# Kernel optimization log

Measured on AMD Instinct MI355X. Metric: run time of the kernel, lower is better.

The kernel has to match this reference:

```python
import jax, jax.numpy as jnp
import numpy as np

B, N, K, C = 4, 4096, 32, 192  # batch, npoint, nsample, channels (C % 6 == 0)
EPS = 1e-5


def setup_inputs() -> dict:
    key = jax.random.key(0)
    ks = jax.random.split(key, 8)
    p = jax.random.normal(ks[0], (B, N, 3), jnp.float32)
    x = jax.random.normal(ks[1], (B, C, N), jnp.float32)
    idx = jax.random.randint(ks[2], (B, N, K), 0, N)  # ball-query neighbor ids
    W = jax.random.normal(ks[3], (C, C + 3), jnp.float32) * 0.05  # 1x1 conv weight
    gamma = 1.0 + 0.1 * jax.random.normal(ks[4], (C,), jnp.float32)
    beta = 0.1 * jax.random.normal(ks[5], (C,), jnp.float32)
    rmean = 0.1 * jax.random.normal(ks[6], (C,), jnp.float32)
    rvar = jax.random.uniform(ks[7], (C,), jnp.float32) + 0.5  # positive running var
    return dict(p=p, x=x, idx=idx, W=W, gamma=gamma, beta=beta, rmean=rmean, rvar=rvar)


def reference(p, x, idx, W, gamma, beta, rmean, rvar):
    # --- grouper: gather neighbors, relative coords ---
    pn = jax.vmap(lambda pp, ii: pp[ii])(p, idx)            # [B,N,K,3]
    dp = jnp.transpose(pn - p[:, :, None, :], (0, 3, 1, 2))  # [B,3,N,K]
    xj = jax.vmap(lambda xx, ii: xx[:, ii])(x, idx)          # [B,C,N,K]
    # --- PosPool sin/cos positional embedding fused with features ---
    feat_dim = C // 6
    dim_mat = jnp.power(500.0, jnp.arange(feat_dim, dtype=jnp.float32) / feat_dim)
    div = (50.0 * dp)[..., None] / dim_mat                   # [B,3,N,K,fd]
    pe = jnp.concatenate([jnp.sin(div), jnp.cos(div)], axis=-1)  # [B,3,N,K,2fd]
    pe = jnp.transpose(pe, (0, 1, 4, 2, 3)).reshape(B, C, N, K)  # [B,C,N,K]
    agg = xj * pe + pe
    # --- dp_fj concat -> 1x1 conv -> BN(eval) -> ReLU ---
    h = jnp.concatenate([dp, agg], axis=1)                   # [B,C+3,N,K]
    y = jnp.einsum('oc,bcnk->bonk', W, h)                    # [B,C,N,K]
    inv = gamma / jnp.sqrt(rvar + EPS)
    y = y * inv[:, None, None] + (beta - rmean * inv)[:, None, None]
    y = jax.nn.relu(y)
    # --- max reduction over neighbors ---
    return jnp.max(y, axis=-1)                               # [B,C,N]
```

## Files before the change

kernel.cpp:

```cpp
#include <hip/hip_runtime.h>
#include <math.h>

#define B_   4
#define N_   4096
#define K_   32
#define C_   192
#define CH_  195
#define KPAD 224
#define PTS  2
#define NKT  7
#define NNT  4
#define GRID ((B_ * N_) / PTS)

using half8  = __attribute__((ext_vector_type(8))) _Float16;
using half2v = __attribute__((ext_vector_type(2))) _Float16;
using f32x4  = __attribute__((ext_vector_type(4))) float;

__device__ _Float16 g_Wp[C_ * KPAD];
__device__ _Float16 g_xT[(size_t)B_ * N_ * C_];

__device__ __forceinline__ float dpp_max16(float v) {
    int s;
    s = __builtin_amdgcn_update_dpp(0, __float_as_int(v), 0xB1,  0xF, 0xF, true);
    v = fmaxf(v, __int_as_float(s));
    s = __builtin_amdgcn_update_dpp(0, __float_as_int(v), 0x4E,  0xF, 0xF, true);
    v = fmaxf(v, __int_as_float(s));
    s = __builtin_amdgcn_update_dpp(0, __float_as_int(v), 0x141, 0xF, 0xF, true);
    v = fmaxf(v, __int_as_float(s));
    s = __builtin_amdgcn_update_dpp(0, __float_as_int(v), 0x140, 0xF, 0xF, true);
    v = fmaxf(v, __int_as_float(s));
    return v;
}

__global__ __launch_bounds__(256) void prep(const float* __restrict__ x,
                                            const float* __restrict__ W,
                                            const float* __restrict__ gamma_,
                                            const float* __restrict__ rvar) {
    const int tid = threadIdx.x;
    if (blockIdx.x < 512) {
        __shared__ float s[32][201];
        const int b  = blockIdx.x >> 7;
        const int n0 = (blockIdx.x & 127) * 32;
        const int cl = tid >> 3;
        const int n4 = (tid & 7) * 4;
#pragma unroll
        for (int it = 0; it < 6; ++it) {
            const int c = it * 32 + cl;
            const float4 v = *(const float4*)(x + ((size_t)b * C_ + c) * N_ + n0 + n4);
            s[n4 + 0][c] = v.x; s[n4 + 1][c] = v.y; s[n4 + 2][c] = v.z; s[n4 + 3][c] = v.w;
        }
        __syncthreads();
        const int n  = tid >> 3;
        const int og = tid & 7;
#pragma unroll
        for (int it = 0; it < 3; ++it) {
            const int oc = it * 8 + og;
            half8 v;
#pragma unroll
            for (int jj = 0; jj < 8; ++jj) v[jj] = (_Float16)s[n][oc * 8 + jj];
            *(half8*)(g_xT + ((size_t)b * N_ + n0 + n) * C_ + oc * 8) = v;
        }
    } else {
        const int i = (blockIdx.x - 512) * 256 + tid;
        if (i < C_ * KPAD) {
            const int o = i / KPAD, r = i - o * KPAD;
            const float inv = gamma_[o] * rsqrtf(rvar[o] + 1e-5f);
            float v = 0.0f;
            if (r < 3)                  v = W[o * CH_ + r];
            else if (r >= 8 && r < 200) v = W[o * CH_ + 3 + (r - 8)];
            g_Wp[i] = (_Float16)(v * inv);
        }
    }
}

__global__ __launch_bounds__(256, 5) void la_mfma(
    const float* __restrict__ p,
    const int*   __restrict__ idx,
    const float* __restrict__ gamma_,
    const float* __restrict__ beta_,
    const float* __restrict__ rmean,
    const float* __restrict__ rvar,
    float* __restrict__ out)
{
    __shared__ _Float16 hb[NKT * NNT * 64 * 8];
    __shared__ float s_bias[C_], s_fr[32];

    const int tid  = threadIdx.x;
    const int lane = tid & 63;
    const int w    = tid >> 6;
    const int l15  = lane & 15;
    const int quad = lane >> 4;

    const int q  = blockIdx.x & 7;
    const int sI = blockIdx.x >> 3;
    const int L  = q * (GRID / 8) + sI;
    const int bn0 = L * PTS;
    const int b   = bn0 >> 12;
    const int n0  = bn0 & (N_ - 1);

    if (tid < C_) {
        const float inv = gamma_[tid] * rsqrtf(rvar[tid] + 1e-5f);
        s_bias[tid] = beta_[tid] - rmean[tid] * inv;
    }
    if (tid < 32) s_fr[tid] = 7.9577471546f * exp2f(-(float)tid * 0.2801808715263400f);
    __syncthreads();

    {
        const int col = w * 16 + l15;
        const int pt  = col >> 5;
        const int k   = col & 31;
        const int gp  = bn0 + pt;
        const int j   = idx[(size_t)gp * K_ + k];
        const float d0 = p[(size_t)(b * N_ + j) * 3 + 0] - p[(size_t)gp * 3 + 0];
        const float d1 = p[(size_t)(b * N_ + j) * 3 + 1] - p[(size_t)gp * 3 + 1];
        const float d2 = p[(size_t)(b * N_ + j) * 3 + 2] - p[(size_t)gp * 3 + 2];
        const _Float16* xh = g_xT + ((size_t)b * N_ + j) * C_;

        float sfr[8];
#pragma unroll
        for (int jj = 0; jj < 8; ++jj) sfr[jj] = s_fr[quad * 8 + jj];

#pragma unroll
        for (int i6 = 0; i6 < 6; ++i6) {
            const int chunk = quad + 4 * i6;
            const half8 v = *(const half8*)(xh + chunk * 8);
            const float dd  = (chunk < 8) ? d0 : ((chunk < 16) ? d1 : d2);
            const float off = (chunk & 4) ? 0.25f : 0.0f;
            half8 hv;
#pragma unroll
            for (int jj = 0; jj < 8; jj += 2) {
                const float pe0 = __builtin_amdgcn_sinf(fmaf(dd, sfr[jj],     off));
                const float pe1 = __builtin_amdgcn_sinf(fmaf(dd, sfr[jj + 1], off));
                const half2v pe2 = __builtin_bit_cast(half2v, __builtin_amdgcn_cvt_pkrtz(pe0, pe1));
                half2v v2; v2[0] = v[jj]; v2[1] = v[jj + 1];
                const half2v r2 = pe2 * v2 + pe2;
                hv[jj] = r2[0]; hv[jj + 1] = r2[1];
            }
            const int ro = chunk + 1;
            const int kt = ro >> 2, kq = ro & 3;
            *(half8*)(&hb[(size_t)((kt * NNT + w) * 64 + kq * 16 + l15) * 8]) = hv;
        }
        if (quad == 0) {
            half8 hv0 = (half8)(_Float16)0.0f;
            hv0[0] = (_Float16)d0; hv0[1] = (_Float16)d1; hv0[2] = (_Float16)d2;
            *(half8*)(&hb[(size_t)((0 * NNT + w) * 64 + 0 * 16 + l15) * 8]) = hv0;
        } else {
            const int ro = 24 + quad;
            const int kt = ro >> 2, kq = ro & 3;
            *(half8*)(&hb[(size_t)((kt * NNT + w) * 64 + kq * 16 + l15) * 8]) = (half8)(_Float16)0.0f;
        }
    }
    __syncthreads();

    f32x4 acc[3][4];
#pragma unroll
    for (int i = 0; i < 3; ++i)
#pragma unroll
        for (int t = 0; t < 4; ++t) acc[i][t] = (f32x4)0.0f;

#pragma unroll
    for (int kt = 0; kt < NKT; ++kt) {
        const int k0 = kt * 32 + quad * 8;
        half8 a[3], bf[4];
#pragma unroll
        for (int i = 0; i < 3; ++i) {
            const int m = (w * 3 + i) * 16 + l15;
            a[i] = *(const half8*)(g_Wp + (size_t)m * KPAD + k0);
        }
#pragma unroll
        for (int t = 0; t < 4; ++t)
            bf[t] = *(const half8*)(&hb[(size_t)((kt * NNT + t) * 64 + lane) * 8]);
#pragma unroll
        for (int i = 0; i < 3; ++i)
#pragma unroll
            for (int t = 0; t < 4; ++t)
                acc[i][t] = __builtin_amdgcn_mfma_f32_16x16x32_f16(a[i], bf[t], acc[i][t], 0, 0, 0);
    }

#pragma unroll
    for (int i = 0; i < 3; ++i) {
        const int mbase = (w * 3 + i) * 16 + quad * 4;
#pragma unroll
        for (int r = 0; r < 4; ++r) {
            float v0 = fmaxf(acc[i][0][r], acc[i][1][r]);
            float v1 = fmaxf(acc[i][2][r], acc[i][3][r]);
            v0 = dpp_max16(v0);
            v1 = dpp_max16(v1);
            if (l15 == 0) {
                const int m = mbase + r;
                const float bias = s_bias[m];
                float2 o2;
                o2.x = fmaxf(v0 + bias, 0.0f);
                o2.y = fmaxf(v1 + bias, 0.0f);
                *(float2*)(&out[((size_t)b * C_ + m) * N_ + n0]) = o2;
            }
        }
    }
}

extern "C" void kernel_launch(void* const* d_in, const int* in_sizes, int n_in,
                              void* d_out, int out_size, void* d_ws, size_t ws_size,
                              hipStream_t stream) {
    (void)in_sizes; (void)n_in; (void)out_size; (void)d_ws; (void)ws_size;
    const float* p      = (const float*)d_in[0];
    const float* x      = (const float*)d_in[1];
    const int*   idx    = (const int*)d_in[2];
    const float* W      = (const float*)d_in[3];
    const float* gamma_ = (const float*)d_in[4];
    const float* beta_  = (const float*)d_in[5];
    const float* rmean  = (const float*)d_in[6];
    const float* rvar   = (const float*)d_in[7];
    float* out = (float*)d_out;

    prep<<<512 + (C_ * KPAD + 255) / 256, 256, 0, stream>>>(x, W, gamma_, rvar);
    la_mfma<<<GRID, 256, 0, stream>>>(p, idx, gamma_, beta_, rmean, rvar, out);
}
```

Baseline: 179.7 us.

## Split K-dimension into two LDS phases to shrink shared memory and raise occupancy

The B-operand staging buffer is cut to hold only four K-tiles. The first 16 channel chunks are built and consumed by MFMA, then the buffer is reused for the remaining chunks plus the dp coordinates, which now sit at the end of the reordered weight layout. Launch bounds rise from 5 to 8 waves per SIMD hint to exploit the smaller LDS footprint. The epilogue stages results in shared memory so one coalesced float2 store per channel replaces per-lane writes. The cost is two extra barriers and a serialized build/compute phase within each block.

```diff
diff --git a/kernel.cpp b/kernel.cpp
--- a/kernel.cpp
+++ b/kernel.cpp
@@ -9,6 +9,7 @@
 #define KPAD 224
 #define PTS  2
 #define NKT  7
+#define NKT0 4
 #define NNT  4
 #define GRID ((B_ * N_) / PTS)
 
@@ -66,14 +67,14 @@
             const int o = i / KPAD, r = i - o * KPAD;
             const float inv = gamma_[o] * rsqrtf(rvar[o] + 1e-5f);
             float v = 0.0f;
-            if (r < 3)                  v = W[o * CH_ + r];
-            else if (r >= 8 && r < 200) v = W[o * CH_ + 3 + (r - 8)];
+            if (r < 192)      v = W[o * CH_ + 3 + r];
+            else if (r < 195) v = W[o * CH_ + (r - 192)];
             g_Wp[i] = (_Float16)(v * inv);
         }
     }
 }
 
-__global__ __launch_bounds__(256, 5) void la_mfma(
+__global__ __launch_bounds__(256, 8) void la_mfma(
     const float* __restrict__ p,
     const int*   __restrict__ idx,
     const float* __restrict__ gamma_,
@@ -82,8 +83,8 @@
     const float* __restrict__ rvar,
     float* __restrict__ out)
 {
-    __shared__ _Float16 hb[NKT * NNT * 64 * 8];
-    __shared__ float s_bias[C_], s_fr[32];
+    __shared__ _Float16 hb[NKT0 * NNT * 64 * 8];
+    __shared__ float s_bias[C_], s_fr[32], s_out[C_ * PTS];
 
     const int tid  = threadIdx.x;
     const int lane = tid & 63;
@@ -105,52 +106,40 @@
     if (tid < 32) s_fr[tid] = 7.9577471546f * exp2f(-(float)tid * 0.2801808715263400f);
     __syncthreads();
 
-    {
-        const int col = w * 16 + l15;
-        const int pt  = col >> 5;
-        const int k   = col & 31;
-        const int gp  = bn0 + pt;
-        const int j   = idx[(size_t)gp * K_ + k];
-        const float d0 = p[(size_t)(b * N_ + j) * 3 + 0] - p[(size_t)gp * 3 + 0];
-        const float d1 = p[(size_t)(b * N_ + j) * 3 + 1] - p[(size_t)gp * 3 + 1];
-        const float d2 = p[(size_t)(b * N_ + j) * 3 + 2] - p[(size_t)gp * 3 + 2];
-        const _Float16* xh = g_xT + ((size_t)b * N_ + j) * C_;
-
-        float sfr[8];
-#pragma unroll
-        for (int jj = 0; jj < 8; ++jj) sfr[jj] = s_fr[quad * 8 + jj];
-
-#pragma unroll
-        for (int i6 = 0; i6 < 6; ++i6) {
-            const int chunk = quad + 4 * i6;
-            const half8 v = *(const half8*)(xh + chunk * 8);
-            const float dd  = (chunk < 8) ? d0 : ((chunk < 16) ? d1 : d2);
-            const float off = (chunk & 4) ? 0.25f : 0.0f;
-            half8 hv;
-#pragma unroll
-            for (int jj = 0; jj < 8; jj += 2) {
-                const float pe0 = __builtin_amdgcn_sinf(fmaf(dd, sfr[jj],     off));
-                const float pe1 = __builtin_amdgcn_sinf(fmaf(dd, sfr[jj + 1], off));
-                const half2v pe2 = __builtin_bit_cast(half2v, __builtin_amdgcn_cvt_pkrtz(pe0, pe1));
-                half2v v2; v2[0] = v[jj]; v2[1] = v[jj + 1];
-                const half2v r2 = pe2 * v2 + pe2;
-                hv[jj] = r2[0]; hv[jj + 1] = r2[1];
-            }
-            const int ro = chunk + 1;
-            const int kt = ro >> 2, kq = ro & 3;
-            *(half8*)(&hb[(size_t)((kt * NNT + w) * 64 + kq * 16 + l15) * 8]) = hv;
-        }
-        if (quad == 0) {
-            half8 hv0 = (half8)(_Float16)0.0f;
-            hv0[0] = (_Float16)d0; hv0[1] = (_Float16)d1; hv0[2] = (_Float16)d2;
-            *(half8*)(&hb[(size_t)((0 * NNT + w) * 64 + 0 * 16 + l15) * 8]) = hv0;
-        } else {
-            const int ro = 24 + quad;
-            const int kt = ro >> 2, kq = ro & 3;
-            *(half8*)(&hb[(size_t)((kt * NNT + w) * 64 + kq * 16 + l15) * 8]) = (half8)(_Float16)0.0f;
-        }
-    }
-    __syncthreads();
+    const int col = w * 16 + l15;
+    const int pt  = col >> 5;
+    const int k   = col & 31;
+    const int gp  = bn0 + pt;
+    const int j   = idx[(size_t)gp * K_ + k];
+    const float d0 = p[(size_t)(b * N_ + j) * 3 + 0] - p[(size_t)gp * 3 + 0];
+    const float d1 = p[(size_t)(b * N_ + j) * 3 + 1] - p[(size_t)gp * 3 + 1];
+    const float d2 = p[(size_t)(b * N_ + j) * 3 + 2] - p[(size_t)gp * 3 + 2];
+    const _Float16* xh = g_xT + ((size_t)b * N_ + j) * C_;
+
+    float sfr[8];
+#pragma unroll
+    for (int jj = 0; jj < 8; ++jj) sfr[jj] = s_fr[quad * 8 + jj];
+
+    auto emit_chunk = [&](int i6) {
+        const int chunk = quad + 4 * i6;
+        const half8 v = *(const half8*)(xh + chunk * 8);
+        const float dd  = (chunk < 8) ? d0 : ((chunk < 16) ? d1 : d2);
+        const float off = (chunk & 4) ? 0.25f : 0.0f;
+        half8 hv;
+#pragma unroll
+        for (int jj = 0; jj < 8; jj += 2) {
+            const float pe0 = __builtin_amdgcn_sinf(fmaf(dd, sfr[jj],     off));
+            const float pe1 = __builtin_amdgcn_sinf(fmaf(dd, sfr[jj + 1], off));
+            const half2v pe2 = __builtin_bit_cast(half2v, __builtin_amdgcn_cvt_pkrtz(pe0, pe1));
+            half2v v2; v2[0] = v[jj]; v2[1] = v[jj + 1];
+            const half2v r2 = pe2 * v2 + pe2;
+            hv[jj] = r2[0]; hv[jj + 1] = r2[1];
+        }
+        const int kt  = chunk >> 2;
+        const int kq  = chunk & 3;
+        const int lkt = (chunk >= 16) ? (kt - NKT0) : kt;
+        *(half8*)(&hb[(size_t)((lkt * NNT + w) * 64 + kq * 16 + l15) * 8]) = hv;
+    };
 
     f32x4 acc[3][4];
 #pragma unroll
@@ -159,7 +148,11 @@
         for (int t = 0; t < 4; ++t) acc[i][t] = (f32x4)0.0f;
 
 #pragma unroll
-    for (int kt = 0; kt < NKT; ++kt) {
+    for (int i6 = 0; i6 < 4; ++i6) emit_chunk(i6);
+    __syncthreads();
+
+#pragma unroll
+    for (int kt = 0; kt < NKT0; ++kt) {
         const int k0 = kt * 32 + quad * 8;
         half8 a[3], bf[4];
 #pragma unroll
@@ -176,25 +169,61 @@
             for (int t = 0; t < 4; ++t)
                 acc[i][t] = __builtin_amdgcn_mfma_f32_16x16x32_f16(a[i], bf[t], acc[i][t], 0, 0, 0);
     }
+    __syncthreads();
+
+#pragma unroll
+    for (int i6 = 4; i6 < 6; ++i6) emit_chunk(i6);
+    if (quad == 0) {
+        half8 hv0 = (half8)(_Float16)0.0f;
+        hv0[0] = (_Float16)d0; hv0[1] = (_Float16)d1; hv0[2] = (_Float16)d2;
+        *(half8*)(&hb[(size_t)((2 * NNT + w) * 64 + 0 * 16 + l15) * 8]) = hv0;
+    } else {
+        *(half8*)(&hb[(size_t)((2 * NNT + w) * 64 + quad * 16 + l15) * 8]) = (half8)(_Float16)0.0f;
+    }
+    __syncthreads();
+
+#pragma unroll
+    for (int kt = NKT0; kt < NKT; ++kt) {
+        const int k0 = kt * 32 + quad * 8;
+        half8 a[3], bf[4];
+#pragma unroll
+        for (int i = 0; i < 3; ++i) {
+            const int m = (w * 3 + i) * 16 + l15;
+            a[i] = *(const half8*)(g_Wp + (size_t)m * KPAD + k0);
+        }
+#pragma unroll
+        for (int t = 0; t < 4; ++t)
+            bf[t] = *(const half8*)(&hb[(size_t)(((kt - NKT0) * NNT + t) * 64 + lane) * 8]);
+#pragma unroll
+        for (int i = 0; i < 3; ++i)
+#pragma unroll
+            for (int t = 0; t < 4; ++t)
+                acc[i][t] = __builtin_amdgcn_mfma_f32_16x16x32_f16(a[i], bf[t], acc[i][t], 0, 0, 0);
+    }
 
 #pragma unroll
     for (int i = 0; i < 3; ++i) {
         const int mbase = (w * 3 + i) * 16 + quad * 4;
 #pragma unroll
-        for (int r = 0; r < 4; ++r) {
-            float v0 = fmaxf(acc[i][0][r], acc[i][1][r]);
-            float v1 = fmaxf(acc[i][2][r], acc[i][3][r]);
-            v0 = dpp_max16(v0);
-            v1 = dpp_max16(v1);
-            if (l15 == 0) {
-                const int m = mbase + r;
-                const float bias = s_bias[m];
-                float2 o2;
-                o2.x = fmaxf(v0 + bias, 0.0f);
-                o2.y = fmaxf(v1 + bias, 0.0f);
-                *(float2*)(&out[((size_t)b * C_ + m) * N_ + n0]) = o2;
+        for (int ptc = 0; ptc < PTS; ++ptc) {
+            const f32x4 va = acc[i][2 * ptc];
+            const f32x4 vb = acc[i][2 * ptc + 1];
+#pragma unroll
+            for (int r = 0; r < 4; ++r) {
+                float v = fmaxf(va[r], vb[r]);
+                v = dpp_max16(v);
+                if (l15 == 0) {
+                    const int m = mbase + r;
+                    s_out[m * PTS + ptc] = fmaxf(v + s_bias[m], 0.0f);
+                }
             }
         }
+    }
+    __syncthreads();
+
+    if (tid < C_) {
+        const float2 o2 = *(const float2*)(&s_out[tid * PTS]);
+        *(float2*)(&out[((size_t)b * C_ + tid) * N_ + n0]) = o2;
     }
 }
 
```

Measured after the change: 598.7 us. 233% more time.

## Swap MFMA operands, reorder K layout, stage outputs through shared memory

Applied to the files above, without the earlier changes.

The MFMA A/B operands are swapped so each lane's accumulator holds neighbor rows of one output channel. The max over neighbors can then be done mostly in-register with two cross-quad shuffles instead of a 4-step DPP reduction per row. The packed weight and LDS K layout are reordered to put the features first and the dp coordinates last. All six feature loads are hoisted ahead of the sin computation to increase memory-level parallelism. Output goes to shared memory and is written by 192 threads after an extra barrier, at the cost of a little more LDS and one more sync.

```diff
diff --git a/kernel.cpp b/kernel.cpp
--- a/kernel.cpp
+++ b/kernel.cpp
@@ -18,19 +18,6 @@
 
 __device__ _Float16 g_Wp[C_ * KPAD];
 __device__ _Float16 g_xT[(size_t)B_ * N_ * C_];
-
-__device__ __forceinline__ float dpp_max16(float v) {
-    int s;
-    s = __builtin_amdgcn_update_dpp(0, __float_as_int(v), 0xB1,  0xF, 0xF, true);
-    v = fmaxf(v, __int_as_float(s));
-    s = __builtin_amdgcn_update_dpp(0, __float_as_int(v), 0x4E,  0xF, 0xF, true);
-    v = fmaxf(v, __int_as_float(s));
-    s = __builtin_amdgcn_update_dpp(0, __float_as_int(v), 0x141, 0xF, 0xF, true);
-    v = fmaxf(v, __int_as_float(s));
-    s = __builtin_amdgcn_update_dpp(0, __float_as_int(v), 0x140, 0xF, 0xF, true);
-    v = fmaxf(v, __int_as_float(s));
-    return v;
-}
 
 __global__ __launch_bounds__(256) void prep(const float* __restrict__ x,
                                             const float* __restrict__ W,
@@ -66,8 +53,8 @@
             const int o = i / KPAD, r = i - o * KPAD;
             const float inv = gamma_[o] * rsqrtf(rvar[o] + 1e-5f);
             float v = 0.0f;
-            if (r < 3)                  v = W[o * CH_ + r];
-            else if (r >= 8 && r < 200) v = W[o * CH_ + 3 + (r - 8)];
+            if (r < 192)      v = W[o * CH_ + 3 + r];
+            else if (r < 195) v = W[o * CH_ + (r - 192)];
             g_Wp[i] = (_Float16)(v * inv);
         }
     }
@@ -83,7 +70,7 @@
     float* __restrict__ out)
 {
     __shared__ _Float16 hb[NKT * NNT * 64 * 8];
-    __shared__ float s_bias[C_], s_fr[32];
+    __shared__ float s_bias[C_], s_fr[32], s_out[C_ * PTS];
 
     const int tid  = threadIdx.x;
     const int lane = tid & 63;
@@ -116,6 +103,11 @@
         const float d2 = p[(size_t)(b * N_ + j) * 3 + 2] - p[(size_t)gp * 3 + 2];
         const _Float16* xh = g_xT + ((size_t)b * N_ + j) * C_;
 
+        half8 v6[6];
+#pragma unroll
+        for (int i6 = 0; i6 < 6; ++i6)
+            v6[i6] = *(const half8*)(xh + (quad + 4 * i6) * 8);
+
         float sfr[8];
 #pragma unroll
         for (int jj = 0; jj < 8; ++jj) sfr[jj] = s_fr[quad * 8 + jj];
@@ -123,7 +115,7 @@
 #pragma unroll
         for (int i6 = 0; i6 < 6; ++i6) {
             const int chunk = quad + 4 * i6;
-            const half8 v = *(const half8*)(xh + chunk * 8);
+            const half8 v = v6[i6];
             const float dd  = (chunk < 8) ? d0 : ((chunk < 16) ? d1 : d2);
             const float off = (chunk & 4) ? 0.25f : 0.0f;
             half8 hv;
@@ -136,18 +128,15 @@
                 const half2v r2 = pe2 * v2 + pe2;
                 hv[jj] = r2[0]; hv[jj + 1] = r2[1];
             }
-            const int ro = chunk + 1;
-            const int kt = ro >> 2, kq = ro & 3;
-            *(half8*)(&hb[(size_t)((kt * NNT + w) * 64 + kq * 16 + l15) * 8]) = hv;
+            const int kt = chunk >> 2;
+            *(half8*)(&hb[(size_t)((kt * NNT + w) * 64 + quad * 16 + l15) * 8]) = hv;
         }
         if (quad == 0) {
             half8 hv0 = (half8)(_Float16)0.0f;
             hv0[0] = (_Float16)d0; hv0[1] = (_Float16)d1; hv0[2] = (_Float16)d2;
-            *(half8*)(&hb[(size_t)((0 * NNT + w) * 64 + 0 * 16 + l15) * 8]) = hv0;
+            *(half8*)(&hb[(size_t)((6 * NNT + w) * 64 + 0 * 16 + l15) * 8]) = hv0;
         } else {
-            const int ro = 24 + quad;
-            const int kt = ro >> 2, kq = ro & 3;
-            *(half8*)(&hb[(size_t)((kt * NNT + w) * 64 + kq * 16 + l15) * 8]) = (half8)(_Float16)0.0f;
+            *(half8*)(&hb[(size_t)((6 * NNT + w) * 64 + quad * 16 + l15) * 8]) = (half8)(_Float16)0.0f;
         }
     }
     __syncthreads();
@@ -174,27 +163,36 @@
         for (int i = 0; i < 3; ++i)
 #pragma unroll
             for (int t = 0; t < 4; ++t)
-                acc[i][t] = __builtin_amdgcn_mfma_f32_16x16x32_f16(a[i], bf[t], acc[i][t], 0, 0, 0);
+                acc[i][t] = __builtin_amdgcn_mfma_f32_16x16x32_f16(bf[t], a[i], acc[i][t], 0, 0, 0);
     }
 
 #pragma unroll
     for (int i = 0; i < 3; ++i) {
-        const int mbase = (w * 3 + i) * 16 + quad * 4;
-#pragma unroll
-        for (int r = 0; r < 4; ++r) {
-            float v0 = fmaxf(acc[i][0][r], acc[i][1][r]);
-            float v1 = fmaxf(acc[i][2][r], acc[i][3][r]);
-            v0 = dpp_max16(v0);
-            v1 = dpp_max16(v1);
-            if (l15 == 0) {
-                const int m = mbase + r;
-                const float bias = s_bias[m];
-                float2 o2;
-                o2.x = fmaxf(v0 + bias, 0.0f);
-                o2.y = fmaxf(v1 + bias, 0.0f);
-                *(float2*)(&out[((size_t)b * C_ + m) * N_ + n0]) = o2;
-            }
-        }
+        const int m = (w * 3 + i) * 16 + l15;
+        float vv[PTS];
+#pragma unroll
+        for (int ptc = 0; ptc < PTS; ++ptc) {
+            const f32x4 va = acc[i][2 * ptc];
+            const f32x4 vb = acc[i][2 * ptc + 1];
+            float v = fmaxf(fmaxf(fmaxf(va[0], va[1]), fmaxf(va[2], va[3])),
+                            fmaxf(fmaxf(vb[0], vb[1]), fmaxf(vb[2], vb[3])));
+            v = fmaxf(v, __shfl_xor(v, 16, 64));
+            v = fmaxf(v, __shfl_xor(v, 32, 64));
+            vv[ptc] = v;
+        }
+        if (quad == 0) {
+            const float bias = s_bias[m];
+            float2 o2;
+            o2.x = fmaxf(vv[0] + bias, 0.0f);
+            o2.y = fmaxf(vv[1] + bias, 0.0f);
+            *(float2*)(&s_out[m * PTS]) = o2;
+        }
+    }
+    __syncthreads();
+
+    if (tid < C_) {
+        const float2 o2 = *(const float2*)(&s_out[tid * PTS]);
+        *(float2*)(&out[((size_t)b * C_ + tid) * N_ + n0]) = o2;
     }
 }
 
```

After: 162.8 us. -9.4%, faster.
